# Performance work log

Measured on AMD Instinct MI355X. Metric: run time of the kernel, lower is better.

Reference implementation:

```python
import jax, jax.numpy as jnp
import numpy as np

B, S, E, H = 2, 4096, 512, 8
DK = E // H


def setup_inputs() -> dict:
    k = jax.random.key(0)
    ks = jax.random.split(k, 11)
    sc = 0.02
    return {
        "query": jax.random.normal(ks[0], (B, S, E), jnp.float32),
        "key_in": jax.random.normal(ks[1], (B, S, E), jnp.float32),
        "value": jax.random.normal(ks[2], (B, S, E), jnp.float32),
        "Wq": jax.random.normal(ks[3], (E, E), jnp.float32) * sc,
        "bq": jax.random.normal(ks[4], (E,), jnp.float32) * sc,
        "Wk": jax.random.normal(ks[5], (E, E), jnp.float32) * sc,
        "bk": jax.random.normal(ks[6], (E,), jnp.float32) * sc,
        "Wv": jax.random.normal(ks[7], (E, E), jnp.float32) * sc,
        "bv": jax.random.normal(ks[8], (E,), jnp.float32) * sc,
        "Wo": jax.random.normal(ks[9], (E, E), jnp.float32) * sc,
        "bo": jax.random.normal(ks[10], (E,), jnp.float32) * sc,
    }


def reference(query, key_in, value, Wq, bq, Wk, bk, Wv, bv, Wo, bo):
    b, s, _ = query.shape
    # Linear projections
    q = query @ Wq + bq
    k = key_in @ Wk + bk
    v = value @ Wv + bv
    # [b, s, H, dk] -> [b, H, s, dk]
    q = q.reshape(b, s, H, DK).transpose(0, 2, 1, 3)
    k = k.reshape(b, s, H, DK).transpose(0, 2, 1, 3)
    v = v.reshape(b, s, H, DK).transpose(0, 2, 1, 3)
    # NOTE: source bug — softmax over UNSCALED scores (1/sqrt scaling in the
    # original is applied to a dead variable after softmax). Reproduce faithfully.
    scores = jnp.einsum("bhqd,bhkd->bhqk", q, k)  # [b,H,s,s] — O(N^2) materialized
    weights = jax.nn.softmax(scores.astype(jnp.float32), axis=-1)
    attn = jnp.einsum("bhqk,bhkd->bhqd", weights, v)
    # [b,H,s,dk] -> [b,s,E]
    concat = attn.transpose(0, 2, 1, 3).reshape(b, s, E)
    return concat @ Wo + bo
```

## Files before the change

kernel.cpp:

```cpp
#include <hip/hip_runtime.h>
#include <hip/hip_bf16.h>

#define B_  2
#define S_  4096
#define E_  512
#define H_  8
#define DK_ 64
#define M_  8192

typedef float f32x4  __attribute__((ext_vector_type(4)));
typedef float f32x16 __attribute__((ext_vector_type(16)));
typedef short s16x8  __attribute__((ext_vector_type(8)));
typedef short s16x4  __attribute__((ext_vector_type(4)));

static __device__ __forceinline__ short f2bf(float x) {
  __hip_bfloat16 h = __float2bfloat16(x);
  return __builtin_bit_cast(short, h);
}

static __device__ __forceinline__ f32x4 mfma32(s16x8 a, s16x8 b, f32x4 c) {
  return __builtin_amdgcn_mfma_f32_16x16x32_bf16(a, b, c, 0, 0, 0);
}

static __device__ __forceinline__ f32x16 mfma3232(s16x8 a, s16x8 b, f32x16 c) {
  return __builtin_amdgcn_mfma_f32_32x32x16_bf16(a, b, c, 0, 0, 0);
}

static __device__ __forceinline__ float fastexp2(float x) {
#if __has_builtin(__builtin_amdgcn_exp2f)
  return __builtin_amdgcn_exp2f(x);
#else
  return __expf(x * 0.69314718056f);
#endif
}

static __device__ __forceinline__ void gload_lds16(const void* g, void* l) {
  __builtin_amdgcn_global_load_lds(
      (const __attribute__((address_space(1))) unsigned int*)g,
      (__attribute__((address_space(3))) unsigned int*)l, 16, 0, 0);
}

__global__ __launch_bounds__(256) void conv_bf16_all(
    const float* __restrict__ q, const float* __restrict__ k,
    const float* __restrict__ v, short* __restrict__ out, int n4) {
  const float* in = (blockIdx.y == 0) ? q : ((blockIdx.y == 1) ? k : v);
  short* o = out + (size_t)blockIdx.y * (size_t)n4 * 4;
  int i = blockIdx.x * 256 + threadIdx.x;
  if (i < n4) {
    float4 x = *((const float4*)in + i);
    s16x4 r;
    r[0] = f2bf(x.x); r[1] = f2bf(x.y); r[2] = f2bf(x.z); r[3] = f2bf(x.w);
    *((s16x4*)o + i) = r;
  }
}

__global__ __launch_bounds__(256) void conv_wT_all(
    const float* __restrict__ Wq, const float* __restrict__ Wk,
    const float* __restrict__ Wv, const float* __restrict__ Wo,
    short* __restrict__ Wt) {
  const float* W = (blockIdx.y == 0) ? Wq
                   : ((blockIdx.y == 1) ? Wk : ((blockIdx.y == 2) ? Wv : Wo));
  short* o = Wt + (size_t)blockIdx.y * (E_ * E_);
  int idx = blockIdx.x * 256 + threadIdx.x;
  int j = idx >> 9, k = idx & 511;
  o[idx] = f2bf(W[(size_t)k * E_ + j]);
}

static __device__ __forceinline__ void gemm_core_512(
    const short* __restrict__ A, const short* __restrict__ Bt,
    short* As, short* Bs, int tm, int tn, f32x4 acc[4][4]) {
  const int tid = threadIdx.x;
  const int wave = tid >> 6, lane = tid & 63;
  const int c = lane & 15, g = lane >> 4;
  int fOff[2];
#pragma unroll
  for (int r = 0; r < 2; ++r) {
    const int f = wave * 2 + r;
    fOff[r] = ((f >> 2) * 64 + (f & 3) * 16 + c) * 512 + g * 8;
  }
  auto stg = [&](int p, int b) {
#pragma unroll
    for (int r = 0; r < 2; ++r) {
      const int f = wave * 2 + r;
      gload_lds16(A + (size_t)tm * 512 + p * 32 + fOff[r],
                  (char*)As + b * 8192 + f * 1024);
      gload_lds16(Bt + (size_t)tn * 512 + p * 32 + fOff[r],
                  (char*)Bs + b * 8192 + f * 1024);
    }
  };
  stg(0, 0);
  __syncthreads();
  for (int p = 0; p < 16; ++p) {
    if (p + 1 < 16) stg(p + 1, (p + 1) & 1);
    const short* Ac = As + (p & 1) * 4096;
    const short* Bc = Bs + (p & 1) * 4096;
    s16x8 af[4], bfr[4];
#pragma unroll
    for (int i = 0; i < 4; ++i)
      af[i] = *(const s16x8*)(Ac + ((wave >> 1) * 4 + i) * 512 + lane * 8);
#pragma unroll
    for (int j = 0; j < 4; ++j)
      bfr[j] = *(const s16x8*)(Bc + ((wave & 1) * 4 + j) * 512 + lane * 8);
#pragma unroll
    for (int i = 0; i < 4; ++i)
#pragma unroll
      for (int j = 0; j < 4; ++j)
        acc[i][j] = mfma32(af[i], bfr[j], acc[i][j]);
    __syncthreads();
  }
}

__global__ __launch_bounds__(256) void gemm_qkv(
    const short* __restrict__ Xq, const short* __restrict__ Xk,
    const short* __restrict__ Xv, const short* __restrict__ Wt,
    const float* __restrict__ bq, const float* __restrict__ bk,
    const float* __restrict__ bv,
    short* __restrict__ Qo, short* __restrict__ Ko, short* __restrict__ Vto) {
  __shared__ __align__(16) short As[2 * 4096];
  __shared__ __align__(16) short Bs[2 * 4096];
  const int z = blockIdx.z;
  const short* A = (z == 0) ? Xq : ((z == 1) ? Xk : Xv);
  const short* Bt = Wt + z * (E_ * E_);
  const float* bias = (z == 0) ? bq : ((z == 1) ? bk : bv);
  const int tm = blockIdx.x * 128, tn = blockIdx.y * 128;
  f32x4 acc[4][4] = {};
  gemm_core_512(A, Bt, As, Bs, tm, tn, acc);

  const int tid = threadIdx.x;
  const int wave = tid >> 6, lane = tid & 63;
  const int wm = (wave >> 1) * 64, wn = (wave & 1) * 64;
  const int c = lane & 15, g = lane >> 4;
#pragma unroll
  for (int i = 0; i < 4; ++i) {
#pragma unroll
    for (int j = 0; j < 4; ++j) {
      const int gc = tn + wn + j * 16 + c;
      const float bb = bias[gc];
      const int h = gc >> 6, dk = gc & 63;
      if (z == 2) {
        const int gr0 = tm + wm + i * 16 + g * 4;
        const int b = gr0 >> 12, s0 = gr0 & 4095;
        s16x4 v4;
#pragma unroll
        for (int r = 0; r < 4; ++r) v4[r] = f2bf(acc[i][j][r] + bb);
        *(s16x4*)&Vto[(size_t)((b * H_ + h) * DK_ + dk) * S_ + s0] = v4;
      } else {
#pragma unroll
        for (int r = 0; r < 4; ++r) {
          const int gr = tm + wm + i * 16 + g * 4 + r;
          const int b = gr >> 12, s = gr & 4095;
          float v = acc[i][j][r] + bb;
          if (z == 0) v *= 1.44269504f;
          const short hv = f2bf(v);
          if (z == 1)
            Ko[(size_t)((b * H_ + h) * S_ + s) * DK_ + dk] = hv;
          else
            Qo[(size_t)((b * H_ + h) * S_ + s) * DK_ + dk] = hv;
        }
      }
    }
  }
}

__global__ __launch_bounds__(256) void gemm_out(
    const short* __restrict__ AO, const short* __restrict__ Wot,
    const float* __restrict__ bo, float* __restrict__ out) {
  __shared__ __align__(16) short As[2 * 4096];
  __shared__ __align__(16) short Bs[2 * 4096];
  const int tm = blockIdx.x * 128, tn = blockIdx.y * 128;
  f32x4 acc[4][4] = {};
  gemm_core_512(AO, Wot, As, Bs, tm, tn, acc);

  const int tid = threadIdx.x;
  const int wave = tid >> 6, lane = tid & 63;
  const int wm = (wave >> 1) * 64, wn = (wave & 1) * 64;
  const int c = lane & 15, g = lane >> 4;
#pragma unroll
  for (int i = 0; i < 4; ++i) {
#pragma unroll
    for (int j = 0; j < 4; ++j) {
      const int gc = tn + wn + j * 16 + c;
      const float bb = bo[gc];
#pragma unroll
      for (int r = 0; r < 4; ++r) {
        const int gr = tm + wm + i * 16 + g * 4 + r;
        out[(size_t)gr * E_ + gc] = acc[i][j][r] + bb;
      }
    }
  }
}

__global__ __launch_bounds__(512, 2) void attn_fwd(
    const short* __restrict__ Q, const short* __restrict__ K,
    const short* __restrict__ Vt, short* __restrict__ O) {
  __shared__ __align__(16) char lds[49152];
  const int tid = threadIdx.x;
  const int wave = tid >> 6, lane = tid & 63;
  const int g = wave >> 1, kh = wave & 1;
  const int qi = lane & 31, hi = lane >> 5;
  const int bh = blockIdx.y;
  const int b = bh >> 3, h = bh & 7;
  const int q0 = blockIdx.x * 256 + g * 64;
  const short* Qp = Q + (size_t)bh * S_ * DK_;
  const short* Kp = K + (size_t)bh * S_ * DK_;
  const short* Vp = Vt + (size_t)bh * DK_ * S_;

  s16x8 qfL[4], qfH[4];
#pragma unroll
  for (int s = 0; s < 4; ++s) {
    qfL[s] = *(const s16x8*)(Qp + (size_t)(q0 + qi) * DK_ + s * 16 + hi * 8);
    qfH[s] = *(const s16x8*)(Qp + (size_t)(q0 + 32 + qi) * DK_ + s * 16 + hi * 8);
  }

  f32x16 o00 = {}, o01 = {}, o10 = {}, o11 = {};
  float lsL = 0.f, lsH = 0.f;

  int kOff, vOff;
  {
    const int j = wave;
    const int row = (j >> 2) * 32 + qi;
    const int srow = (row & 32) | ((row & 8) << 1) | ((row & 4) << 1) |
                     ((row & 16) >> 2) | (row & 3);
    kOff = srow * DK_ + (j & 3) * 16 + hi * 8;
    vOff = ((j >> 2) * 32 + qi) * S_ + ((j >> 1) & 1) * 32 +
           (j & 1) * 16 + hi * 8;
  }

  auto stage = [&](int kt) {
    gload_lds16(Kp + (size_t)kt * 64 * DK_ + kOff,
                lds + (kt % 3) * 8192 + wave * 1024);
    gload_lds16(Vp + (size_t)kt * 64 + vOff,
                lds + 24576 + (kt % 3) * 8192 + wave * 1024);
  };

  auto bar2 = [&]() {
    asm volatile("s_waitcnt vmcnt(2) lgkmcnt(0)" ::: "memory");
    __builtin_amdgcn_s_barrier();
  };
  auto bar0 = [&]() {
    asm volatile("s_waitcnt vmcnt(0) lgkmcnt(0)" ::: "memory");
    __builtin_amdgcn_s_barrier();
  };

  const int lbK = kh * 4096 + (lane << 4);

  auto qk = [&](int t, f32x16& sL, f32x16& sH) {
    const char* Kc = lds + (t % 3) * 8192 + lbK;
    f32x16 a = {}, c = {};
    __builtin_amdgcn_s_setprio(1);
#pragma unroll
    for (int s = 0; s < 4; ++s) {
      s16x8 ka = *(const s16x8*)(Kc + s * 1024);
      a = mfma3232(ka, qfL[s], a);
      c = mfma3232(ka, qfH[s], c);
    }
    __builtin_amdgcn_s_setprio(0);
    sL = a; sH = c;
  };

  auto softpv = [&](const f32x16& sL, const f32x16& sH, int t) {
    const char* Vc = lds + 24576 + (t % 3) * 8192 + kh * 2048 + (lane << 4);
    float pL[16], pH[16];
#pragma unroll
    for (int r = 0; r < 16; ++r) { pL[r] = fastexp2(sL[r]); pH[r] = fastexp2(sH[r]); }
    float aL = 0.f, aH = 0.f;
#pragma unroll
    for (int r = 0; r < 16; ++r) { aL += pL[r]; aH += pH[r]; }
    lsL += aL; lsH += aH;
    s16x8 pbL[2], pbH[2];
#pragma unroll
    for (int ks = 0; ks < 2; ++ks)
#pragma unroll
      for (int j = 0; j < 8; ++j) {
        const int r = (j & 3) | (ks << 2) | ((j >> 2) << 3);
        pbL[ks][j] = f2bf(pL[r]);
        pbH[ks][j] = f2bf(pH[r]);
      }
    __builtin_amdgcn_s_setprio(1);
#pragma unroll
    for (int ks = 0; ks < 2; ++ks) {
      s16x8 va0 = *(const s16x8*)(Vc + ks * 1024);
      s16x8 va1 = *(const s16x8*)(Vc + 4096 + ks * 1024);
      o00 = mfma3232(va0, pbL[ks], o00);
      o01 = mfma3232(va0, pbH[ks], o01);
      o10 = mfma3232(va1, pbL[ks], o10);
      o11 = mfma3232(va1, pbH[ks], o11);
    }
    __builtin_amdgcn_s_setprio(0);
  };

  const int NT = S_ / 64;
  f32x16 sA0, sA1, sB0, sB1;

  stage(0);
  stage(1);
  bar2();
  qk(0, sA0, sA1);

  for (int t = 0; t < NT; t += 2) {
    if (t + 2 < NT) { stage(t + 2); bar2(); } else { bar0(); }
    qk(t + 1, sB0, sB1);
    softpv(sA0, sA1, t);
    if (t + 3 < NT) { stage(t + 3); bar2(); } else { bar0(); }
    if (t + 2 < NT) qk(t + 2, sA0, sA1);
    softpv(sB0, sB1, t + 1);
  }

  lsL += __shfl_xor(lsL, 32);
  lsH += __shfl_xor(lsH, 32);

  float* mrg = (float*)lds;
  const int mi = (g * 64 + lane) * 36;
  __syncthreads();
  if (kh) {
#pragma unroll
    for (int r = 0; r < 4; ++r) {
      *(f32x4*)(mrg + mi + r * 4) =
          f32x4{o00[r * 4], o00[r * 4 + 1], o00[r * 4 + 2], o00[r * 4 + 3]};
      *(f32x4*)(mrg + mi + 16 + r * 4) =
          f32x4{o01[r * 4], o01[r * 4 + 1], o01[r * 4 + 2], o01[r * 4 + 3]};
    }
    mrg[mi + 32] = lsL;
    mrg[mi + 33] = lsH;
  }
  __syncthreads();
  float rlL = 0.f, rlH = 0.f;
  if (!kh) {
#pragma unroll
    for (int r = 0; r < 16; ++r) {
      o00[r] += mrg[mi + r];
      o01[r] += mrg[mi + 16 + r];
    }
    rlL = 1.f / (lsL + mrg[mi + 32]);
    rlH = 1.f / (lsH + mrg[mi + 33]);
  }
  __syncthreads();
  if (kh) {
#pragma unroll
    for (int r = 0; r < 4; ++r) {
      *(f32x4*)(mrg + mi + r * 4) =
          f32x4{o10[r * 4], o10[r * 4 + 1], o10[r * 4 + 2], o10[r * 4 + 3]};
      *(f32x4*)(mrg + mi + 16 + r * 4) =
          f32x4{o11[r * 4], o11[r * 4 + 1], o11[r * 4 + 2], o11[r * 4 + 3]};
    }
  }
  __syncthreads();
  if (!kh) {
#pragma unroll
    for (int r = 0; r < 16; ++r) {
      o10[r] += mrg[mi + r];
      o11[r] += mrg[mi + 16 + r];
    }
    short* OpL = O + ((size_t)(b * S_ + q0 + qi)) * E_ + h * DK_;
    short* OpH = O + ((size_t)(b * S_ + q0 + 32 + qi)) * E_ + h * DK_;
#pragma unroll
    for (int rr = 0; rr < 4; ++rr) {
      s16x4 vL0, vL1, vH0, vH1;
#pragma unroll
      for (int e = 0; e < 4; ++e) {
        vL0[e] = f2bf(o00[rr * 4 + e] * rlL);
        vL1[e] = f2bf(o10[rr * 4 + e] * rlL);
        vH0[e] = f2bf(o01[rr * 4 + e] * rlH);
        vH1[e] = f2bf(o11[rr * 4 + e] * rlH);
      }
      *(s16x4*)(OpL + rr * 8 + hi * 4) = vL0;
      *(s16x4*)(OpL + 32 + rr * 8 + hi * 4) = vL1;
      *(s16x4*)(OpH + rr * 8 + hi * 4) = vH0;
      *(s16x4*)(OpH + 32 + rr * 8 + hi * 4) = vH1;
    }
  }
}

extern "C" void kernel_launch(void* const* d_in, const int* in_sizes, int n_in,
                              void* d_out, int out_size, void* d_ws, size_t ws_size,
                              hipStream_t stream) {
  const float* query  = (const float*)d_in[0];
  const float* key_in = (const float*)d_in[1];
  const float* value  = (const float*)d_in[2];
  const float* Wq = (const float*)d_in[3];
  const float* bq = (const float*)d_in[4];
  const float* Wk = (const float*)d_in[5];
  const float* bk = (const float*)d_in[6];
  const float* Wv = (const float*)d_in[7];
  const float* bv = (const float*)d_in[8];
  const float* Wo = (const float*)d_in[9];
  const float* bo = (const float*)d_in[10];
  float* out = (float*)d_out;

  const size_t NA = (size_t)M_ * E_;
  short* ws  = (short*)d_ws;
  short* Xq  = ws;
  short* Wt  = Xq + 3 * NA;
  short* Wot = Wt + 3 * E_ * E_;
  short* Qb  = Wt + 4 * E_ * E_;
  short* Kb  = Qb + NA;
  short* Vtb = Kb + NA;
  short* AO  = Vtb + NA;
  short* Xk  = Xq + NA;
  short* Xv  = Xk + NA;

  conv_bf16_all<<<dim3(NA / 1024, 3), 256, 0, stream>>>(
      query, key_in, value, Xq, (int)(NA / 4));
  conv_wT_all<<<dim3(E_ * E_ / 256, 4), 256, 0, stream>>>(Wq, Wk, Wv, Wo, Wt);

  gemm_qkv<<<dim3(M_ / 128, E_ / 128, 3), 256, 0, stream>>>(
      Xq, Xk, Xv, Wt, bq, bk, bv, Qb, Kb, Vtb);
  attn_fwd<<<dim3(S_ / 256, B_ * H_), 512, 0, stream>>>(Qb, Kb, Vtb, AO);
  gemm_out<<<dim3(M_ / 128, E_ / 128), 256, 0, stream>>>(AO, Wot, bo, out);
}
```

Baseline: 148.0 us.

## Load K/V tiles directly into registers instead of staging through LDS

Removes the triple-buffered LDS staging of K and V tiles, along with the barriers around it. Each wave now loads its K and V MFMA operands straight from global memory into registers, double-buffered in registers across iterations. This drops LDS traffic and block-wide synchronisation, but every wave now issues its own global loads, with less coalescing and more register pressure. LDS is kept only for the final merge of the two key halves.

```diff
diff --git a/kernel.cpp b/kernel.cpp
--- a/kernel.cpp
+++ b/kernel.cpp
@@ -193,7 +193,7 @@
 __global__ __launch_bounds__(512, 2) void attn_fwd(
     const short* __restrict__ Q, const short* __restrict__ K,
     const short* __restrict__ Vt, short* __restrict__ O) {
-  __shared__ __align__(16) char lds[49152];
+  __shared__ __align__(16) float mrg[9216];
   const int tid = threadIdx.x;
   const int wave = tid >> 6, lane = tid & 63;
   const int g = wave >> 1, kh = wave & 1;
@@ -215,101 +215,95 @@
   f32x16 o00 = {}, o01 = {}, o10 = {}, o11 = {};
   float lsL = 0.f, lsH = 0.f;
 
-  int kOff, vOff;
-  {
-    const int j = wave;
-    const int row = (j >> 2) * 32 + qi;
-    const int srow = (row & 32) | ((row & 8) << 1) | ((row & 4) << 1) |
-                     ((row & 16) >> 2) | (row & 3);
-    kOff = srow * DK_ + (j & 3) * 16 + hi * 8;
-    vOff = ((j >> 2) * 32 + qi) * S_ + ((j >> 1) & 1) * 32 +
-           (j & 1) * 16 + hi * 8;
-  }
-
-  auto stage = [&](int kt) {
-    gload_lds16(Kp + (size_t)kt * 64 * DK_ + kOff,
-                lds + (kt % 3) * 8192 + wave * 1024);
-    gload_lds16(Vp + (size_t)kt * 64 + vOff,
-                lds + 24576 + (kt % 3) * 8192 + wave * 1024);
-  };
-
-  auto bar2 = [&]() {
-    asm volatile("s_waitcnt vmcnt(2) lgkmcnt(0)" ::: "memory");
-    __builtin_amdgcn_s_barrier();
-  };
-  auto bar0 = [&]() {
-    asm volatile("s_waitcnt vmcnt(0) lgkmcnt(0)" ::: "memory");
-    __builtin_amdgcn_s_barrier();
-  };
-
-  const int lbK = kh * 4096 + (lane << 4);
-
-  auto qk = [&](int t, f32x16& sL, f32x16& sH) {
-    const char* Kc = lds + (t % 3) * 8192 + lbK;
-    f32x16 a = {}, c = {};
-    __builtin_amdgcn_s_setprio(1);
-#pragma unroll
-    for (int s = 0; s < 4; ++s) {
-      s16x8 ka = *(const s16x8*)(Kc + s * 1024);
-      a = mfma3232(ka, qfL[s], a);
-      c = mfma3232(ka, qfH[s], c);
-    }
-    __builtin_amdgcn_s_setprio(0);
-    sL = a; sH = c;
-  };
-
-  auto softpv = [&](const f32x16& sL, const f32x16& sH, int t) {
-    const char* Vc = lds + 24576 + (t % 3) * 8192 + kh * 2048 + (lane << 4);
-    float pL[16], pH[16];
-#pragma unroll
-    for (int r = 0; r < 16; ++r) { pL[r] = fastexp2(sL[r]); pH[r] = fastexp2(sH[r]); }
-    float aL = 0.f, aH = 0.f;
-#pragma unroll
-    for (int r = 0; r < 16; ++r) { aL += pL[r]; aH += pH[r]; }
-    lsL += aL; lsH += aH;
-    s16x8 pbL[2], pbH[2];
-#pragma unroll
-    for (int ks = 0; ks < 2; ++ks)
-#pragma unroll
-      for (int j = 0; j < 8; ++j) {
-        const int r = (j & 3) | (ks << 2) | ((j >> 2) << 3);
-        pbL[ks][j] = f2bf(pL[r]);
-        pbH[ks][j] = f2bf(pH[r]);
-      }
-    __builtin_amdgcn_s_setprio(1);
-#pragma unroll
-    for (int ks = 0; ks < 2; ++ks) {
-      s16x8 va0 = *(const s16x8*)(Vc + ks * 1024);
-      s16x8 va1 = *(const s16x8*)(Vc + 4096 + ks * 1024);
-      o00 = mfma3232(va0, pbL[ks], o00);
-      o01 = mfma3232(va0, pbH[ks], o01);
-      o10 = mfma3232(va1, pbL[ks], o10);
-      o11 = mfma3232(va1, pbH[ks], o11);
-    }
-    __builtin_amdgcn_s_setprio(0);
-  };
+  const int row = kh * 32 + qi;
+  const int srow = (row & 32) | ((row & 8) << 1) | ((row & 4) << 1) |
+                   ((row & 16) >> 2) | (row & 3);
+  const int kBase = srow * DK_ + hi * 8;
+  const int vBase0 = qi * S_ + kh * 32 + hi * 8;
+  const int vBase1 = (32 + qi) * S_ + kh * 32 + hi * 8;
+
+#define LOADK(t, k0, k1, k2, k3)                                       \
+  {                                                                    \
+    const short* kp_ = Kp + (size_t)(t) * 64 * DK_ + kBase;            \
+    k0 = *(const s16x8*)(kp_);                                         \
+    k1 = *(const s16x8*)(kp_ + 16);                                    \
+    k2 = *(const s16x8*)(kp_ + 32);                                    \
+    k3 = *(const s16x8*)(kp_ + 48);                                    \
+  }
+#define LOADV(t, v0, v1, v2, v3)                                       \
+  {                                                                    \
+    const short* vp_ = Vp + (size_t)(t) * 64;                          \
+    v0 = *(const s16x8*)(vp_ + vBase0);                                \
+    v1 = *(const s16x8*)(vp_ + vBase0 + 16);                           \
+    v2 = *(const s16x8*)(vp_ + vBase1);                                \
+    v3 = *(const s16x8*)(vp_ + vBase1 + 16);                           \
+  }
+
+#define QK(k0, k1, k2, k3, sL, sH)                                     \
+  {                                                                    \
+    f32x16 a_ = {}, c_ = {};                                           \
+    __builtin_amdgcn_s_setprio(1);                                     \
+    a_ = mfma3232(k0, qfL[0], a_); c_ = mfma3232(k0, qfH[0], c_);      \
+    a_ = mfma3232(k1, qfL[1], a_); c_ = mfma3232(k1, qfH[1], c_);      \
+    a_ = mfma3232(k2, qfL[2], a_); c_ = mfma3232(k2, qfH[2], c_);      \
+    a_ = mfma3232(k3, qfL[3], a_); c_ = mfma3232(k3, qfH[3], c_);      \
+    __builtin_amdgcn_s_setprio(0);                                     \
+    sL = a_; sH = c_;                                                  \
+  }
+
+#define SOFTPV(sL, sH, v0, v1, v2, v3)                                 \
+  {                                                                    \
+    float pL_[16], pH_[16];                                            \
+    _Pragma("unroll")                                                  \
+    for (int r = 0; r < 16; ++r) {                                     \
+      pL_[r] = fastexp2((sL)[r]);                                      \
+      pH_[r] = fastexp2((sH)[r]);                                      \
+    }                                                                  \
+    float aL_ = 0.f, aH_ = 0.f;                                        \
+    _Pragma("unroll")                                                  \
+    for (int r = 0; r < 16; ++r) { aL_ += pL_[r]; aH_ += pH_[r]; }     \
+    lsL += aL_; lsH += aH_;                                            \
+    s16x8 pbL_[2], pbH_[2];                                            \
+    _Pragma("unroll")                                                  \
+    for (int ks = 0; ks < 2; ++ks)                                     \
+      _Pragma("unroll")                                                \
+      for (int j = 0; j < 8; ++j) {                                    \
+        const int r = (j & 3) | (ks << 2) | ((j >> 2) << 3);           \
+        pbL_[ks][j] = f2bf(pL_[r]);                                    \
+        pbH_[ks][j] = f2bf(pH_[r]);                                    \
+      }                                                                \
+    __builtin_amdgcn_s_setprio(1);                                     \
+    o00 = mfma3232(v0, pbL_[0], o00); o01 = mfma3232(v0, pbH_[0], o01);\
+    o10 = mfma3232(v2, pbL_[0], o10); o11 = mfma3232(v2, pbH_[0], o11);\
+    o00 = mfma3232(v1, pbL_[1], o00); o01 = mfma3232(v1, pbH_[1], o01);\
+    o10 = mfma3232(v3, pbL_[1], o10); o11 = mfma3232(v3, pbH_[1], o11);\
+    __builtin_amdgcn_s_setprio(0);                                     \
+  }
+
+  s16x8 kA0, kA1, kA2, kA3, vA0, vA1, vA2, vA3;
+  s16x8 kB0, kB1, kB2, kB3, vB0, vB1, vB2, vB3;
+  f32x16 sL, sH;
+
+  LOADK(0, kA0, kA1, kA2, kA3);
+  LOADV(0, vA0, vA1, vA2, vA3);
 
   const int NT = S_ / 64;
-  f32x16 sA0, sA1, sB0, sB1;
-
-  stage(0);
-  stage(1);
-  bar2();
-  qk(0, sA0, sA1);
-
   for (int t = 0; t < NT; t += 2) {
-    if (t + 2 < NT) { stage(t + 2); bar2(); } else { bar0(); }
-    qk(t + 1, sB0, sB1);
-    softpv(sA0, sA1, t);
-    if (t + 3 < NT) { stage(t + 3); bar2(); } else { bar0(); }
-    if (t + 2 < NT) qk(t + 2, sA0, sA1);
-    softpv(sB0, sB1, t + 1);
+    LOADK(t + 1, kB0, kB1, kB2, kB3);
+    LOADV(t + 1, vB0, vB1, vB2, vB3);
+    QK(kA0, kA1, kA2, kA3, sL, sH);
+    SOFTPV(sL, sH, vA0, vA1, vA2, vA3);
+    if (t + 2 < NT) {
+      LOADK(t + 2, kA0, kA1, kA2, kA3);
+      LOADV(t + 2, vA0, vA1, vA2, vA3);
+    }
+    QK(kB0, kB1, kB2, kB3, sL, sH);
+    SOFTPV(sL, sH, vB0, vB1, vB2, vB3);
   }
 
   lsL += __shfl_xor(lsL, 32);
   lsH += __shfl_xor(lsH, 32);
 
-  float* mrg = (float*)lds;
   const int mi = (g * 64 + lane) * 36;
   __syncthreads();
   if (kh) {
@@ -369,6 +363,10 @@
       *(s16x4*)(OpH + 32 + rr * 8 + hi * 4) = vH1;
     }
   }
+#undef LOADK
+#undef LOADV
+#undef QK
+#undef SOFTPV
 }
 
 extern "C" void kernel_launch(void* const* d_in, const int* in_sizes, int n_in,
```

Result: slower. 189.1 us (+27.8%).

## Fuse fp32-to-bf16 input conversion into QKV GEMM and halve attention block size

Applied to the files above, without the earlier changes.

Drops the separate kernel that converted query/key/value to bf16. The QKV GEMM now loads fp32 A tiles into registers, converts them and writes them to LDS, prefetching the next tile while the current one is used. This removes an extra pass over the activations through global memory. It also changes attention to 256-thread blocks covering 128 queries each, with each wave staging two K/V fragments and waiting on a matching count, so twice as many blocks are launched and each stages K/V for fewer queries.

```diff
diff --git a/kernel.cpp b/kernel.cpp
--- a/kernel.cpp
+++ b/kernel.cpp
@@ -38,20 +38,6 @@
   __builtin_amdgcn_global_load_lds(
       (const __attribute__((address_space(1))) unsigned int*)g,
       (__attribute__((address_space(3))) unsigned int*)l, 16, 0, 0);
-}
-
-__global__ __launch_bounds__(256) void conv_bf16_all(
-    const float* __restrict__ q, const float* __restrict__ k,
-    const float* __restrict__ v, short* __restrict__ out, int n4) {
-  const float* in = (blockIdx.y == 0) ? q : ((blockIdx.y == 1) ? k : v);
-  short* o = out + (size_t)blockIdx.y * (size_t)n4 * 4;
-  int i = blockIdx.x * 256 + threadIdx.x;
-  if (i < n4) {
-    float4 x = *((const float4*)in + i);
-    s16x4 r;
-    r[0] = f2bf(x.x); r[1] = f2bf(x.y); r[2] = f2bf(x.z); r[3] = f2bf(x.w);
-    *((s16x4*)o + i) = r;
-  }
 }
 
 __global__ __launch_bounds__(256) void conv_wT_all(
@@ -110,21 +96,82 @@
   }
 }
 
+static __device__ __forceinline__ void gemm_core_f32A(
+    const float* __restrict__ A, const short* __restrict__ Bt,
+    short* As, short* Bs, int tm, int tn, f32x4 acc[4][4]) {
+  const int tid = threadIdx.x;
+  const int wave = tid >> 6, lane = tid & 63;
+  const int c = lane & 15, g = lane >> 4;
+  int fOff[2];
+#pragma unroll
+  for (int r = 0; r < 2; ++r) {
+    const int f = wave * 2 + r;
+    fOff[r] = ((f >> 2) * 64 + (f & 3) * 16 + c) * 512 + g * 8;
+  }
+  auto stgB = [&](int p, int b) {
+#pragma unroll
+    for (int r = 0; r < 2; ++r)
+      gload_lds16(Bt + (size_t)tn * 512 + p * 32 + fOff[r],
+                  (char*)Bs + b * 8192 + (wave * 2 + r) * 1024);
+  };
+  float4 a0[2], a1[2];
+  auto ldA = [&](int p) {
+#pragma unroll
+    for (int r = 0; r < 2; ++r) {
+      const float* ap = A + (size_t)tm * 512 + p * 32 + fOff[r];
+      a0[r] = *(const float4*)ap;
+      a1[r] = *(const float4*)(ap + 4);
+    }
+  };
+  auto wrA = [&](int b) {
+#pragma unroll
+    for (int r = 0; r < 2; ++r) {
+      s16x8 w;
+      w[0] = f2bf(a0[r].x); w[1] = f2bf(a0[r].y);
+      w[2] = f2bf(a0[r].z); w[3] = f2bf(a0[r].w);
+      w[4] = f2bf(a1[r].x); w[5] = f2bf(a1[r].y);
+      w[6] = f2bf(a1[r].z); w[7] = f2bf(a1[r].w);
+      *(s16x8*)((char*)As + b * 8192 + (wave * 2 + r) * 1024 + lane * 16) = w;
+    }
+  };
+  ldA(0); stgB(0, 0); wrA(0);
+  __syncthreads();
+  for (int p = 0; p < 16; ++p) {
+    if (p + 1 < 16) { ldA(p + 1); stgB(p + 1, (p + 1) & 1); }
+    const short* Ac = As + (p & 1) * 4096;
+    const short* Bc = Bs + (p & 1) * 4096;
+    s16x8 af[4], bfr[4];
+#pragma unroll
+    for (int i = 0; i < 4; ++i)
+      af[i] = *(const s16x8*)(Ac + ((wave >> 1) * 4 + i) * 512 + lane * 8);
+#pragma unroll
+    for (int j = 0; j < 4; ++j)
+      bfr[j] = *(const s16x8*)(Bc + ((wave & 1) * 4 + j) * 512 + lane * 8);
+#pragma unroll
+    for (int i = 0; i < 4; ++i)
+#pragma unroll
+      for (int j = 0; j < 4; ++j)
+        acc[i][j] = mfma32(af[i], bfr[j], acc[i][j]);
+    if (p + 1 < 16) wrA((p + 1) & 1);
+    __syncthreads();
+  }
+}
+
 __global__ __launch_bounds__(256) void gemm_qkv(
-    const short* __restrict__ Xq, const short* __restrict__ Xk,
-    const short* __restrict__ Xv, const short* __restrict__ Wt,
+    const float* __restrict__ Xq, const float* __restrict__ Xk,
+    const float* __restrict__ Xv, const short* __restrict__ Wt,
     const float* __restrict__ bq, const float* __restrict__ bk,
     const float* __restrict__ bv,
     short* __restrict__ Qo, short* __restrict__ Ko, short* __restrict__ Vto) {
   __shared__ __align__(16) short As[2 * 4096];
   __shared__ __align__(16) short Bs[2 * 4096];
   const int z = blockIdx.z;
-  const short* A = (z == 0) ? Xq : ((z == 1) ? Xk : Xv);
+  const float* A = (z == 0) ? Xq : ((z == 1) ? Xk : Xv);
   const short* Bt = Wt + z * (E_ * E_);
   const float* bias = (z == 0) ? bq : ((z == 1) ? bk : bv);
   const int tm = blockIdx.x * 128, tn = blockIdx.y * 128;
   f32x4 acc[4][4] = {};
-  gemm_core_512(A, Bt, As, Bs, tm, tn, acc);
+  gemm_core_f32A(A, Bt, As, Bs, tm, tn, acc);
 
   const int tid = threadIdx.x;
   const int wave = tid >> 6, lane = tid & 63;
@@ -190,7 +237,7 @@
   }
 }
 
-__global__ __launch_bounds__(512, 2) void attn_fwd(
+__global__ __launch_bounds__(256, 2) void attn_fwd(
     const short* __restrict__ Q, const short* __restrict__ K,
     const short* __restrict__ Vt, short* __restrict__ O) {
   __shared__ __align__(16) char lds[49152];
@@ -200,7 +247,7 @@
   const int qi = lane & 31, hi = lane >> 5;
   const int bh = blockIdx.y;
   const int b = bh >> 3, h = bh & 7;
-  const int q0 = blockIdx.x * 256 + g * 64;
+  const int q0 = blockIdx.x * 128 + g * 64;
   const short* Qp = Q + (size_t)bh * S_ * DK_;
   const short* Kp = K + (size_t)bh * S_ * DK_;
   const short* Vp = Vt + (size_t)bh * DK_ * S_;
@@ -215,26 +262,31 @@
   f32x16 o00 = {}, o01 = {}, o10 = {}, o11 = {};
   float lsL = 0.f, lsH = 0.f;
 
-  int kOff, vOff;
-  {
-    const int j = wave;
-    const int row = (j >> 2) * 32 + qi;
+  int kOffL[2], vOffL[2];
+#pragma unroll
+  for (int r = 0; r < 2; ++r) {
+    const int f = wave * 2 + r;
+    const int row = (f >> 2) * 32 + qi;
     const int srow = (row & 32) | ((row & 8) << 1) | ((row & 4) << 1) |
                      ((row & 16) >> 2) | (row & 3);
-    kOff = srow * DK_ + (j & 3) * 16 + hi * 8;
-    vOff = ((j >> 2) * 32 + qi) * S_ + ((j >> 1) & 1) * 32 +
-           (j & 1) * 16 + hi * 8;
+    kOffL[r] = srow * DK_ + (f & 3) * 16 + hi * 8;
+    vOffL[r] = ((f >> 2) * 32 + qi) * S_ + ((f >> 1) & 1) * 32 +
+               (f & 1) * 16 + hi * 8;
   }
 
   auto stage = [&](int kt) {
-    gload_lds16(Kp + (size_t)kt * 64 * DK_ + kOff,
-                lds + (kt % 3) * 8192 + wave * 1024);
-    gload_lds16(Vp + (size_t)kt * 64 + vOff,
-                lds + 24576 + (kt % 3) * 8192 + wave * 1024);
-  };
-
-  auto bar2 = [&]() {
-    asm volatile("s_waitcnt vmcnt(2) lgkmcnt(0)" ::: "memory");
+#pragma unroll
+    for (int r = 0; r < 2; ++r) {
+      const int f = wave * 2 + r;
+      gload_lds16(Kp + (size_t)kt * 64 * DK_ + kOffL[r],
+                  lds + (kt % 3) * 8192 + f * 1024);
+      gload_lds16(Vp + (size_t)kt * 64 + vOffL[r],
+                  lds + 24576 + (kt % 3) * 8192 + f * 1024);
+    }
+  };
+
+  auto bar4 = [&]() {
+    asm volatile("s_waitcnt vmcnt(4) lgkmcnt(0)" ::: "memory");
     __builtin_amdgcn_s_barrier();
   };
   auto bar0 = [&]() {
@@ -294,14 +346,14 @@
 
   stage(0);
   stage(1);
-  bar2();
+  bar4();
   qk(0, sA0, sA1);
 
   for (int t = 0; t < NT; t += 2) {
-    if (t + 2 < NT) { stage(t + 2); bar2(); } else { bar0(); }
+    if (t + 2 < NT) { stage(t + 2); bar4(); } else { bar0(); }
     qk(t + 1, sB0, sB1);
     softpv(sA0, sA1, t);
-    if (t + 3 < NT) { stage(t + 3); bar2(); } else { bar0(); }
+    if (t + 3 < NT) { stage(t + 3); bar4(); } else { bar0(); }
     if (t + 2 < NT) qk(t + 2, sA0, sA1);
     softpv(sB0, sB1, t + 1);
   }
@@ -389,22 +441,17 @@
 
   const size_t NA = (size_t)M_ * E_;
   short* ws  = (short*)d_ws;
-  short* Xq  = ws;
-  short* Wt  = Xq + 3 * NA;
+  short* Wt  = ws;
   short* Wot = Wt + 3 * E_ * E_;
   short* Qb  = Wt + 4 * E_ * E_;
   short* Kb  = Qb + NA;
   short* Vtb = Kb + NA;
   short* AO  = Vtb + NA;
-  short* Xk  = Xq + NA;
-  short* Xv  = Xk + NA;
-
-  conv_bf16_all<<<dim3(NA / 1024, 3), 256, 0, stream>>>(
-      query, key_in, value, Xq, (int)(NA / 4));
+
   conv_wT_all<<<dim3(E_ * E_ / 256, 4), 256, 0, stream>>>(Wq, Wk, Wv, Wo, Wt);
 
   gemm_qkv<<<dim3(M_ / 128, E_ / 128, 3), 256, 0, stream>>>(
-      Xq, Xk, Xv, Wt, bq, bk, bv, Qb, Kb, Vtb);
-  attn_fwd<<<dim3(S_ / 256, B_ * H_), 512, 0, stream>>>(Qb, Kb, Vtb, AO);
+      query, key_in, value, Wt, bq, bk, bv, Qb, Kb, Vtb);
+  attn_fwd<<<dim3(S_ / 128, B_ * H_), 256, 0, stream>>>(Qb, Kb, Vtb, AO);
   gemm_out<<<dim3(M_ / 128, E_ / 128), 256, 0, stream>>>(AO, Wot, bo, out);
 }
```

After: 148.2 us. About the same (+0.2%).
